# Performance work log

Hardware: AMD Instinct MI355X
Metric: run time of the kernel (lower is better)

The kernel has to match this reference:

```python
import jax, jax.numpy as jnp
import numpy as np

EMBED = 1024
HIDDEN = 4 * EMBED
EPS = 1e-5

def _layer_norm(x, g, b):
    mu = jnp.mean(x, axis=-1, keepdims=True)
    var = jnp.mean((x - mu) ** 2, axis=-1, keepdims=True)
    return (x - mu) * jax.lax.rsqrt(var + EPS) * g + b

def setup_inputs() -> dict:
    key = jax.random.key(0)
    ks = jax.random.split(key, 8)
    s = 1.0 / np.sqrt(EMBED)
    inp = {
        "x": jax.random.normal(ks[0], (4, 2048, EMBED), dtype=jnp.float32),
        "Wq": jax.random.normal(ks[1], (EMBED, EMBED), dtype=jnp.float32) * s,
        "bq": jnp.zeros((EMBED,), jnp.float32),
        "Wk": jax.random.normal(ks[2], (EMBED, EMBED), dtype=jnp.float32) * s,
        "bk": jnp.zeros((EMBED,), jnp.float32),
        "Wv": jax.random.normal(ks[3], (EMBED, EMBED), dtype=jnp.float32) * s,
        "bv": jnp.zeros((EMBED,), jnp.float32),
        "W1": jax.random.normal(ks[4], (EMBED, HIDDEN), dtype=jnp.float32) * s,
        "b1": jnp.zeros((HIDDEN,), jnp.float32),
        "W2": jax.random.normal(ks[5], (HIDDEN, EMBED), dtype=jnp.float32) * (1.0 / np.sqrt(HIDDEN)),
        "b2": jnp.zeros((EMBED,), jnp.float32),
        "g1": jnp.ones((EMBED,), jnp.float32),
        "be1": jnp.zeros((EMBED,), jnp.float32),
        "g2": jnp.ones((EMBED,), jnp.float32),
        "be2": jnp.zeros((EMBED,), jnp.float32),
    }
    return inp

def reference(x, Wq, bq, Wk, bk, Wv, bv, W1, b1, W2, b2, g1, be1, g2, be2):
    # pre-norm attention
    h = _layer_norm(x, g1, be1)
    Q = h @ Wq + bq  # [B,S,D]
    K = h @ Wk + bk
    V = h @ Wv + bv
    scale = 1.0 / jnp.sqrt(jnp.asarray(EMBED, x.dtype))
    scores = jnp.einsum('bqd,bkd->bqk', Q, K) * scale  # [B,S,S]
    weights = jax.nn.softmax(scores, axis=-1)
    attn = jnp.einsum('bqk,bkd->bqd', weights, V)
    x = x + attn
    # pre-norm MLP
    h2 = _layer_norm(x, g2, be2)
    ff = jax.nn.relu(h2 @ W1 + b1) @ W2 + b2
    return x + ff
```

## Files before the change

### kernel.cpp

```cpp
#include <hip/hip_runtime.h>

#define EMBED 1024
#define HID   4096
#define NB    4
#define SEQ   2048

typedef __attribute__((ext_vector_type(8))) __bf16 bf16x8;
typedef __attribute__((ext_vector_type(4))) float  f32x4;
typedef __attribute__((ext_vector_type(4))) int    i32x4;
typedef unsigned short u16;

__device__ __forceinline__ u16 f2bf(float f) {
  unsigned u = __float_as_uint(f);
  u += 0x7FFFu + ((u >> 16) & 1u);
  return (u16)(u >> 16);
}

typedef const __attribute__((address_space(1))) unsigned int* gas_t;
typedef __attribute__((address_space(3))) unsigned int* las_t;
__device__ __forceinline__ void gld16(const void* g, void* l) {
  __builtin_amdgcn_global_load_lds((gas_t)g, (las_t)l, 16, 0, 0);
}

#define RD16(p)       __builtin_bit_cast(bf16x8, *(const i32x4*)(p))
#define MFMA16(a,b,c) __builtin_amdgcn_mfma_f32_16x16x32_bf16(a, b, c, 0, 0, 0)
#define SCHED0()      __builtin_amdgcn_sched_barrier(0)
#define BARR()        __builtin_amdgcn_s_barrier()
#define LGKM(n)       asm volatile("s_waitcnt lgkmcnt(" #n ")" ::: "memory")
#define VMW(n)        asm volatile("s_waitcnt vmcnt(" #n ")" ::: "memory")

template<int EPI>
__global__ __launch_bounds__(512, 2) void gemm256(
    const u16* __restrict__ A, int lda, long long astr,
    const u16* __restrict__ B, int ldb, long long bstr,
    void* __restrict__ C, int ldc, long long cstr,
    const float* __restrict__ bias,
    const float* __restrict__ add,
    float scale, int Kdim)
{
  __shared__ char lds[131072];

  const int tid  = threadIdx.x;
  const int lane = tid & 63;
  const int w    = tid >> 6;
  const int wr   = w >> 2, wc = w & 3;
  const int l15  = lane & 15, l4 = lane >> 4;

  const int gx   = gridDim.x;
  const int nwg  = gx * gridDim.y;
  const int orig = blockIdx.y * gx + blockIdx.x;
  const int t    = ((nwg & 7) == 0) ? ((orig & 7) * (nwg >> 3) + (orig >> 3)) : orig;
  const int bx   = t % gx, by = t / gx;

  const u16* Ab = A + (size_t)blockIdx.z * astr + (size_t)by * 256 * lda;
  const u16* Bb = B + (size_t)blockIdx.z * bstr + (size_t)bx * 256 * ldb;

  const int    srow = tid >> 3;
  const size_t sa   = (size_t)srow * lda + (size_t)(((tid & 7) ^ (srow & 7)) * 8);
  const size_t sb   = (size_t)srow * ldb + (size_t)(((tid & 7) ^ (srow & 7)) * 8);
  const int    ldst = tid * 16;

  auto stA = [&](int buf, int q, int kk) {
    gld16(Ab + (size_t)(q * 64) * lda + kk + sa, lds + buf * 65536 + q * 8192 + ldst);
  };
  auto stB = [&](int buf, int i, int kk) {
    gld16(Bb + (size_t)(i * 64) * ldb + kk + sb, lds + buf * 65536 + 32768 + i * 8192 + ldst);
  };

  const int arow = (wr * 128 + l15) * 128;
  const int brow = 32768 + (wc * 64 + l15) * 128;
  const int cp0  = ((0 + l4) ^ (l15 & 7)) * 16;
  const int cp1  = ((4 + l4) ^ (l15 & 7)) * 16;

  f32x4 acc[8][4] = {};
  bf16x8 a0, a1, a2, a3, b0, b1, b2, b3, b4, b5, b6, b7;

  const int NT = Kdim >> 6;
  const int NI = NT >> 1;

#define BLOADS(LB) \
    b0 = RD16((LB) + brow + 0 * 2048 + cp0); \
    b1 = RD16((LB) + brow + 1 * 2048 + cp0); \
    b2 = RD16((LB) + brow + 2 * 2048 + cp0); \
    b3 = RD16((LB) + brow + 3 * 2048 + cp0); \
    b4 = RD16((LB) + brow + 0 * 2048 + cp1); \
    b5 = RD16((LB) + brow + 1 * 2048 + cp1); \
    b6 = RD16((LB) + brow + 2 * 2048 + cp1); \
    b7 = RD16((LB) + brow + 3 * 2048 + cp1);

#define PHASE(LB, MP, PRE, STG, VMST) do { \
    a0 = RD16((LB) + arow + (MP) * 4096 + cp0); \
    a1 = RD16((LB) + arow + (MP) * 4096 + cp1); \
    a2 = RD16((LB) + arow + (MP) * 4096 + 2048 + cp0); \
    a3 = RD16((LB) + arow + (MP) * 4096 + 2048 + cp1); \
    PRE STG VMST \
    SCHED0(); BARR(); LGKM(0); SCHED0(); \
    __builtin_amdgcn_s_setprio(1); \
    acc[2*(MP)  ][0] = MFMA16(a0, b0, acc[2*(MP)  ][0]); \
    acc[2*(MP)  ][1] = MFMA16(a0, b1, acc[2*(MP)  ][1]); \
    acc[2*(MP)  ][2] = MFMA16(a0, b2, acc[2*(MP)  ][2]); \
    acc[2*(MP)  ][3] = MFMA16(a0, b3, acc[2*(MP)  ][3]); \
    acc[2*(MP)+1][0] = MFMA16(a2, b0, acc[2*(MP)+1][0]); \
    acc[2*(MP)+1][1] = MFMA16(a2, b1, acc[2*(MP)+1][1]); \
    acc[2*(MP)+1][2] = MFMA16(a2, b2, acc[2*(MP)+1][2]); \
    acc[2*(MP)+1][3] = MFMA16(a2, b3, acc[2*(MP)+1][3]); \
    acc[2*(MP)  ][0] = MFMA16(a1, b4, acc[2*(MP)  ][0]); \
    acc[2*(MP)  ][1] = MFMA16(a1, b5, acc[2*(MP)  ][1]); \
    acc[2*(MP)  ][2] = MFMA16(a1, b6, acc[2*(MP)  ][2]); \
    acc[2*(MP)  ][3] = MFMA16(a1, b7, acc[2*(MP)  ][3]); \
    acc[2*(MP)+1][0] = MFMA16(a3, b4, acc[2*(MP)+1][0]); \
    acc[2*(MP)+1][1] = MFMA16(a3, b5, acc[2*(MP)+1][1]); \
    acc[2*(MP)+1][2] = MFMA16(a3, b6, acc[2*(MP)+1][2]); \
    acc[2*(MP)+1][3] = MFMA16(a3, b7, acc[2*(MP)+1][3]); \
    __builtin_amdgcn_s_setprio(0); \
    SCHED0(); BARR(); SCHED0(); \
  } while (0)

  stB(0, 0, 0); stB(0, 1, 0); stB(0, 2, 0); stB(0, 3, 0);
  stA(0, 0, 0); stA(0, 1, 0); stA(0, 2, 0); stA(0, 3, 0);
  stB(1, 0, 64); stB(1, 1, 64); stB(1, 2, 64); stB(1, 3, 64);
  stA(1, 0, 64); stA(1, 2, 64);
  VMW(6);
  BARR(); SCHED0();

  const char* L0 = lds;
  const char* L1 = lds + 65536;

  for (int I = 0; I < NI; ++I) {
    const bool st = (I + 1 < NI);
    const int k1 = (2 * I + 1) * 64;
    const int k2 = (2 * I + 2) * 64;
    const int k3 = (2 * I + 3) * 64;

    PHASE(L0, 0, BLOADS(L0), { stA(1, 1, k1); stA(1, 3, k1); }, ;);
    PHASE(L0, 1, ;, if (st) { stB(0, 0, k2); stB(0, 1, k2); }, ;);
    PHASE(L0, 2, ;, if (st) { stB(0, 2, k2); stB(0, 3, k2); }, ;);
    if (st) { PHASE(L0, 3, ;, { stA(0, 0, k2); stA(0, 2, k2); }, VMW(6);); }
    else    { PHASE(L0, 3, ;, ;, VMW(0);); }
    PHASE(L1, 0, BLOADS(L1), if (st) { stA(0, 1, k2); stA(0, 3, k2); }, ;);
    PHASE(L1, 1, ;, if (st) { stB(1, 0, k3); stB(1, 1, k3); }, ;);
    PHASE(L1, 2, ;, if (st) { stB(1, 2, k3); stB(1, 3, k3); }, ;);
    if (st) { PHASE(L1, 3, ;, { stA(1, 0, k3); stA(1, 2, k3); }, VMW(6);); }
    else    { PHASE(L1, 3, ;, ;, ;); }
  }
#undef PHASE
#undef BLOADS

  const int bm0 = by * 256 + wr * 128;
  const int bn0 = bx * 256 + wc * 64;
  float* Cf = (float*)C;
  u16*   Ch = (u16*)C;
  #pragma unroll
  for (int mi = 0; mi < 8; ++mi) {
    #pragma unroll
    for (int ni = 0; ni < 4; ++ni) {
      const int col = bn0 + ni * 16 + l15;
      const int r0  = bm0 + mi * 16 + l4 * 4;
      float bv = 0.f;
      if (EPI == 0 || EPI == 3 || EPI == 4) bv = bias[col];
      #pragma unroll
      for (int r = 0; r < 4; ++r) {
        const size_t idx = (size_t)blockIdx.z * cstr + (size_t)(r0 + r) * ldc + col;
        const float v = acc[mi][ni][r];
        if      (EPI == 0) Ch[idx] = f2bf(v + bv);
        else if (EPI == 1) Cf[idx] = v * scale;
        else if (EPI == 3) Ch[idx] = f2bf(fmaxf(v + bv, 0.f));
        else if (EPI == 4) Cf[idx] = v + bv + add[idx];
      }
    }
  }
}

template<int EPI>
__global__ __launch_bounds__(512, 2) void gemm8p(
    const u16* __restrict__ A, int lda, long long astr,
    const u16* __restrict__ B, int ldb, long long bstr,
    void* __restrict__ C, int ldc, long long cstr,
    const float* __restrict__ bias,
    const float* __restrict__ add,
    float scale, int Kdim)
{
  __shared__ i32x4 lds4[9216];
  const int SLOT = 49152;

  const int tid  = threadIdx.x;
  const int lane = tid & 63;
  const int w    = tid >> 6;
  const int wr   = w >> 1, wc = w & 1;
  const int l15  = lane & 15, l4 = lane >> 4;

  const int gx   = gridDim.x;
  const int nwg  = gx * gridDim.y;
  const int orig = blockIdx.y * gx + blockIdx.x;
  const int t    = ((nwg & 7) == 0) ? ((orig & 7) * (nwg >> 3) + (orig >> 3)) : orig;
  const int bx   = t % gx, by = t / gx;

  const u16* Ab = A + (size_t)blockIdx.z * astr + (size_t)by * 256 * lda;
  const u16* Bb = B + (size_t)blockIdx.z * bstr + (size_t)bx * 128 * ldb;

  size_t gaoff[4], gboff[2];
  #pragma unroll
  for (int i = 0; i < 4; ++i) {
    const int idx = i * 512 + tid, row = idx >> 3, gc = (idx & 7) ^ (row & 7);
    gaoff[i] = (size_t)row * lda + gc * 8;
  }
  #pragma unroll
  for (int j = 0; j < 2; ++j) {
    const int idx = j * 512 + tid, row = idx >> 3, gc = (idx & 7) ^ (row & 7);
    gboff[j] = (size_t)row * ldb + gc * 8;
  }

  int aoff[4], boff[4], cp16[2];
  #pragma unroll
  for (int m = 0; m < 4; ++m) aoff[m] = (wr * 64 + m * 16 + l15) * 128;
  #pragma unroll
  for (int n = 0; n < 4; ++n) boff[n] = 32768 + (wc * 64 + n * 16 + l15) * 128;
  cp16[0] = ((0 + l4) ^ (l15 & 7)) * 16;
  cp16[1] = ((4 + l4) ^ (l15 & 7)) * 16;

  f32x4 acc[4][4] = {};
  const int NT = Kdim >> 6;
  char* lbase = (char*)lds4;

  {
    char* s0 = lbase;
    char* s1 = lbase + SLOT;
    #pragma unroll
    for (int i = 0; i < 4; ++i) gld16(Ab + gaoff[i],      s0 + (i * 512 + w * 64) * 16);
    #pragma unroll
    for (int j = 0; j < 2; ++j) gld16(Bb + gboff[j],      s0 + 32768 + (j * 512 + w * 64) * 16);
    #pragma unroll
    for (int i = 0; i < 4; ++i) gld16(Ab + gaoff[i] + 64, s1 + (i * 512 + w * 64) * 16);
    #pragma unroll
    for (int j = 0; j < 2; ++j) gld16(Bb + gboff[j] + 64, s1 + 32768 + (j * 512 + w * 64) * 16);
  }

  int s = 0;
  for (int T = 0; T < NT; ++T) {
    const bool st  = (T + 2 < NT);
    const size_t kk = (size_t)(T + 2) * 64;
    const char* rA = lbase + s * SLOT;
    char* wS = lbase + ((s + 2 >= 3) ? (s - 1) : (s + 2)) * SLOT;

    if (T == NT - 1) VMW(0);
    else             VMW(6);
    BARR();
    SCHED0();

    bf16x8 b0, b1, b2, b3, a0, a1;

    b0 = RD16(rA + boff[0] + cp16[0]);
    b1 = RD16(rA + boff[1] + cp16[0]);
    b2 = RD16(rA + boff[2] + cp16[0]);
    b3 = RD16(rA + boff[3] + cp16[0]);
    a0 = RD16(rA + aoff[0] + cp16[0]);
    a1 = RD16(rA + aoff[1] + cp16[0]);
    if (st) {
      gld16(Ab + gaoff[0] + kk, wS + (0 * 512 + w * 64) * 16);
      gld16(Ab + gaoff[1] + kk, wS + (1 * 512 + w * 64) * 16);
    }
    BARR();
    LGKM(0);
    SCHED0();
    __builtin_amdgcn_s_setprio(1);
    acc[0][0] = MFMA16(a0, b0, acc[0][0]);
    acc[0][1] = MFMA16(a0, b1, acc[0][1]);
    acc[0][2] = MFMA16(a0, b2, acc[0][2]);
    acc[0][3] = MFMA16(a0, b3, acc[0][3]);
    acc[1][0] = MFMA16(a1, b0, acc[1][0]);
    acc[1][1] = MFMA16(a1, b1, acc[1][1]);
    acc[1][2] = MFMA16(a1, b2, acc[1][2]);
    acc[1][3] = MFMA16(a1, b3, acc[1][3]);
    __builtin_amdgcn_s_setprio(0);

    a0 = RD16(rA + aoff[2] + cp16[0]);
    a1 = RD16(rA + aoff[3] + cp16[0]);
    if (st) {
      gld16(Ab + gaoff[2] + kk, wS + (2 * 512 + w * 64) * 16);
      gld16(Ab + gaoff[3] + kk, wS + (3 * 512 + w * 64) * 16);
    }
    BARR();
    LGKM(0);
    SCHED0();
    __builtin_amdgcn_s_setprio(1);
    acc[2][0] = MFMA16(a0, b0, acc[2][0]);
    acc[2][1] = MFMA16(a0, b1, acc[2][1]);
    acc[2][2] = MFMA16(a0, b2, acc[2][2]);
    acc[2][3] = MFMA16(a0, b3, acc[2][3]);
    acc[3][0] = MFMA16(a1, b0, acc[3][0]);
    acc[3][1] = MFMA16(a1, b1, acc[3][1]);
    acc[3][2] = MFMA16(a1, b2, acc[3][2]);
    acc[3][3] = MFMA16(a1, b3, acc[3][3]);
    __builtin_amdgcn_s_setprio(0);

    b0 = RD16(rA + boff[0] + cp16[1]);
    b1 = RD16(rA + boff[1] + cp16[1]);
    b2 = RD16(rA + boff[2] + cp16[1]);
    b3 = RD16(rA + boff[3] + cp16[1]);
    a0 = RD16(rA + aoff[0] + cp16[1]);
    a1 = RD16(rA + aoff[1] + cp16[1]);
    if (st) {
      gld16(Bb + gboff[0] + kk, wS + 32768 + (0 * 512 + w * 64) * 16);
    }
    BARR();
    LGKM(0);
    SCHED0();
    __builtin_amdgcn_s_setprio(1);
    acc[0][0] = MFMA16(a0, b0, acc[0][0]);
    acc[0][1] = MFMA16(a0, b1, acc[0][1]);
    acc[0][2] = MFMA16(a0, b2, acc[0][2]);
    acc[0][3] = MFMA16(a0, b3, acc[0][3]);
    acc[1][0] = MFMA16(a1, b0, acc[1][0]);
    acc[1][1] = MFMA16(a1, b1, acc[1][1]);
    acc[1][2] = MFMA16(a1, b2, acc[1][2]);
    acc[1][3] = MFMA16(a1, b3, acc[1][3]);
    __builtin_amdgcn_s_setprio(0);

    a0 = RD16(rA + aoff[2] + cp16[1]);
    a1 = RD16(rA + aoff[3] + cp16[1]);
    if (st) {
      gld16(Bb + gboff[1] + kk, wS + 32768 + (1 * 512 + w * 64) * 16);
    }
    BARR();
    LGKM(0);
    SCHED0();
    __builtin_amdgcn_s_setprio(1);
    acc[2][0] = MFMA16(a0, b0, acc[2][0]);
    acc[2][1] = MFMA16(a0, b1, acc[2][1]);
    acc[2][2] = MFMA16(a0, b2, acc[2][2]);
    acc[2][3] = MFMA16(a0, b3, acc[2][3]);
    acc[3][0] = MFMA16(a1, b0, acc[3][0]);
    acc[3][1] = MFMA16(a1, b1, acc[3][1]);
    acc[3][2] = MFMA16(a1, b2, acc[3][2]);
    acc[3][3] = MFMA16(a1, b3, acc[3][3]);
    __builtin_amdgcn_s_setprio(0);

    s = (s + 1 == 3) ? 0 : s + 1;
  }

  const int bm0 = by * 256 + wr * 64;
  const int bn0 = bx * 128 + wc * 64;
  float* Cf = (float*)C;
  u16*   Ch = (u16*)C;
  #pragma unroll
  for (int mi = 0; mi < 4; ++mi) {
    #pragma unroll
    for (int ni = 0; ni < 4; ++ni) {
      const int col = bn0 + ni * 16 + l15;
      const int r0  = bm0 + mi * 16 + l4 * 4;
      float bv = 0.f;
      if (EPI == 0 || EPI == 4) bv = bias[col];
      #pragma unroll
      for (int r = 0; r < 4; ++r) {
        const size_t idx = (size_t)blockIdx.z * cstr + (size_t)(r0 + r) * ldc + col;
        const float v = acc[mi][ni][r];
        if      (EPI == 0) Ch[idx] = f2bf(v + bv);
        else if (EPI == 1) Cf[idx] = v * scale;
        else if (EPI == 2) Cf[idx] = v + add[idx];
        else if (EPI == 4) Cf[idx] = v + bv + add[idx];
        else if (EPI == 5) Ch[idx] = f2bf(v + bias[r0 + r]);
      }
    }
  }
}

__global__ __launch_bounds__(256) void ln_kernel(
    const float* __restrict__ x, const float* __restrict__ g,
    const float* __restrict__ be, u16* __restrict__ out)
{
  const int row = blockIdx.x;
  const int tid = threadIdx.x;
  const float4 v = ((const float4*)(x + (size_t)row * EMBED))[tid];
  float s  = v.x + v.y + v.z + v.w;
  float s2 = v.x * v.x + v.y * v.y + v.z * v.z + v.w * v.w;
  #pragma unroll
  for (int m = 1; m < 64; m <<= 1) { s += __shfl_xor(s, m); s2 += __shfl_xor(s2, m); }
  __shared__ float ls[4], ls2[4];
  const int w = tid >> 6;
  if ((tid & 63) == 0) { ls[w] = s; ls2[w] = s2; }
  __syncthreads();
  s  = ls[0] + ls[1] + ls[2] + ls[3];
  s2 = ls2[0] + ls2[1] + ls2[2] + ls2[3];
  const float mu   = s * (1.f / EMBED);
  const float var  = s2 * (1.f / EMBED) - mu * mu;
  const float rstd = rsqrtf(var + 1e-5f);
  const float4 gv = ((const float4*)g)[tid];
  const float4 bv = ((const float4*)be)[tid];
  ushort4 o;
  o.x = f2bf((v.x - mu) * rstd * gv.x + bv.x);
  o.y = f2bf((v.y - mu) * rstd * gv.y + bv.y);
  o.z = f2bf((v.z - mu) * rstd * gv.z + bv.z);
  o.w = f2bf((v.w - mu) * rstd * gv.w + bv.w);
  ((ushort4*)(out + (size_t)row * EMBED))[tid] = o;
}

__global__ __launch_bounds__(256) void softmax_kernel(
    const float* __restrict__ S, u16* __restrict__ P)
{
  const int tid = threadIdx.x;
  const size_t base = ((size_t)blockIdx.y * SEQ + blockIdx.x) * SEQ;
  const float4* src = (const float4*)(S + base);
  float4 a = src[tid];
  float4 b = src[tid + 256];
  float m = fmaxf(fmaxf(fmaxf(a.x, a.y), fmaxf(a.z, a.w)),
                  fmaxf(fmaxf(b.x, b.y), fmaxf(b.z, b.w)));
  #pragma unroll
  for (int msk = 1; msk < 64; msk <<= 1) m = fmaxf(m, __shfl_xor(m, msk));
  __shared__ float red[8];
  const int w = tid >> 6;
  if ((tid & 63) == 0) red[w] = m;
  __syncthreads();
  m = fmaxf(fmaxf(red[0], red[1]), fmaxf(red[2], red[3]));
  a.x = __expf(a.x - m); a.y = __expf(a.y - m); a.z = __expf(a.z - m); a.w = __expf(a.w - m);
  b.x = __expf(b.x - m); b.y = __expf(b.y - m); b.z = __expf(b.z - m); b.w = __expf(b.w - m);
  float s = a.x + a.y + a.z + a.w + b.x + b.y + b.z + b.w;
  #pragma unroll
  for (int msk = 1; msk < 64; msk <<= 1) s += __shfl_xor(s, msk);
  if ((tid & 63) == 0) red[4 + w] = s;
  __syncthreads();
  s = red[4] + red[5] + red[6] + red[7];
  const float inv = 1.0f / s;
  ushort4 oa, ob;
  oa.x = f2bf(a.x * inv); oa.y = f2bf(a.y * inv); oa.z = f2bf(a.z * inv); oa.w = f2bf(a.w * inv);
  ob.x = f2bf(b.x * inv); ob.y = f2bf(b.y * inv); ob.z = f2bf(b.z * inv); ob.w = f2bf(b.w * inv);
  ushort4* dst = (ushort4*)(P + base);
  dst[tid]       = oa;
  dst[tid + 256] = ob;
}

__global__ void transpose_cast_f32(const float* __restrict__ W, u16* __restrict__ Wt,
                                   int K, int N)
{
  __shared__ float t[32][33];
  const int tx = threadIdx.x, ty = threadIdx.y;
  const int n0 = blockIdx.x * 32, k0 = blockIdx.y * 32;
  #pragma unroll
  for (int i = 0; i < 4; ++i)
    t[ty + i * 8][tx] = W[(size_t)(k0 + ty + i * 8) * N + n0 + tx];
  __syncthreads();
  #pragma unroll
  for (int i = 0; i < 4; ++i)
    Wt[(size_t)(n0 + ty + i * 8) * K + k0 + tx] = f2bf(t[tx][ty + i * 8]);
}

__global__ void concat_bias2(const float* __restrict__ a, const float* __restrict__ b,
                             float* __restrict__ o)
{
  const int i = blockIdx.x * 1024 + threadIdx.x;
  o[i] = (i < 1024) ? a[i] : b[i - 1024];
}

extern "C" void kernel_launch(void* const* d_in, const int* in_sizes, int n_in,
                              void* d_out, int out_size, void* d_ws, size_t ws_size,
                              hipStream_t stream)
{
  const float* x   = (const float*)d_in[0];
  const float* Wq  = (const float*)d_in[1];
  const float* bq  = (const float*)d_in[2];
  const float* Wk  = (const float*)d_in[3];
  const float* bk  = (const float*)d_in[4];
  const float* Wv  = (const float*)d_in[5];
  const float* bv  = (const float*)d_in[6];
  const float* W1  = (const float*)d_in[7];
  const float* b1  = (const float*)d_in[8];
  const float* W2  = (const float*)d_in[9];
  const float* b2  = (const float*)d_in[10];
  const float* g1  = (const float*)d_in[11];
  const float* be1 = (const float*)d_in[12];
  const float* g2  = (const float*)d_in[13];
  const float* be2 = (const float*)d_in[14];
  float* out = (float*)d_out;

  const size_t RD = (size_t)NB * SEQ * EMBED;

  char* base = (char*)d_ws;
  size_t o = 0;
  auto alloc = [&](size_t bytes) -> void* {
    o = (o + 255) & ~(size_t)255;
    void* p = base + o;
    o += bytes;
    return p;
  };

  u16*   wqkT = (u16*)alloc((size_t)2 * EMBED * EMBED * 2);
  u16*   wvT  = (u16*)alloc((size_t)EMBED * EMBED * 2);
  u16*   w1T  = (u16*)alloc((size_t)HID * EMBED * 2);
  u16*   w2T  = (u16*)alloc((size_t)EMBED * HID * 2);
  float* bqk  = (float*)alloc(2048 * 4);
  u16*   h    = (u16*)alloc(RD * 2);
  u16*   QKb  = (u16*)alloc(RD * 2 * 2);
  u16*   Vt   = (u16*)alloc(RD * 2);
  float* x2   = (float*)alloc(RD * 4);

  const size_t need_batched = o + (size_t)NB * SEQ * SEQ * 6 + 1024;
  const int NZ = (ws_size >= need_batched) ? NB : 1;
  float* Sbuf = (float*)alloc((size_t)NZ * SEQ * SEQ * 4);
  u16*   Pb   = (u16*)alloc((size_t)NZ * SEQ * SEQ * 2);
  u16*   ff   = (NZ == NB) ? (u16*)Sbuf
                           : (u16*)alloc((size_t)NB * SEQ * HID * 2);

  const dim3 blk(512);
  const dim3 tblk(32, 8);

  transpose_cast_f32<<<dim3(32, 32), tblk, 0, stream>>>(Wq, wqkT, EMBED, EMBED);
  transpose_cast_f32<<<dim3(32, 32), tblk, 0, stream>>>(Wk, wqkT + (size_t)EMBED * EMBED, EMBED, EMBED);
  transpose_cast_f32<<<dim3(32, 32), tblk, 0, stream>>>(Wv, wvT, EMBED, EMBED);
  transpose_cast_f32<<<dim3(HID / 32, EMBED / 32), tblk, 0, stream>>>(W1, w1T, EMBED, HID);
  transpose_cast_f32<<<dim3(EMBED / 32, HID / 32), tblk, 0, stream>>>(W2, w2T, HID, EMBED);
  concat_bias2<<<dim3(2), dim3(1024), 0, stream>>>(bq, bk, bqk);

  ln_kernel<<<dim3(NB * SEQ), dim3(256), 0, stream>>>(x, g1, be1, h);

  gemm8p<0><<<dim3(2048 / 128, NB * SEQ / 256, 1), blk, 0, stream>>>(
      h, EMBED, 0LL, wqkT, EMBED, 0LL, QKb, 2048, 0LL, bqk, nullptr, 1.f, EMBED);

  gemm8p<5><<<dim3(SEQ / 128, EMBED / 256, NB), blk, 0, stream>>>(
      wvT, EMBED, 0LL, h, EMBED, (long long)SEQ * EMBED,
      Vt, SEQ, (long long)EMBED * SEQ, bv, nullptr, 1.f, EMBED);

  for (int b = 0; b < NB; b += NZ) {
    const u16* Qp  = QKb + (size_t)b * SEQ * 2048;
    const u16* Kp  = Qp + 1024;
    const u16* Vtp = Vt + (size_t)b * EMBED * SEQ;
    float* x2p     = x2 + (size_t)b * SEQ * EMBED;
    const float* xp = x + (size_t)b * SEQ * EMBED;
    gemm8p<1><<<dim3(SEQ / 128, SEQ / 256, NZ), blk, 0, stream>>>(
        Qp, 2048, (long long)SEQ * 2048, Kp, 2048, (long long)SEQ * 2048,
        Sbuf, SEQ, (long long)SEQ * SEQ, nullptr, nullptr, 0.03125f, EMBED);
    softmax_kernel<<<dim3(SEQ, NZ), dim3(256), 0, stream>>>(Sbuf, Pb);
    gemm8p<2><<<dim3(EMBED / 128, SEQ / 256, NZ), blk, 0, stream>>>(
        Pb, SEQ, (long long)SEQ * SEQ, Vtp, SEQ, (long long)EMBED * SEQ,
        x2p, EMBED, (long long)SEQ * EMBED, nullptr, xp, 1.f, SEQ);
  }

  ln_kernel<<<dim3(NB * SEQ), dim3(256), 0, stream>>>(x2, g2, be2, h);

  gemm256<3><<<dim3(HID / 256, NB * SEQ / 256, 1), blk, 0, stream>>>(
      h, EMBED, 0LL, w1T, EMBED, 0LL, ff, HID, 0LL, b1, nullptr, 1.f, EMBED);
  gemm8p<4><<<dim3(EMBED / 128, NB * SEQ / 256, 1), blk, 0, stream>>>(
      ff, HID, 0LL, w2T, HID, 0LL, out, EMBED, 0LL, b2, x2, 1.f, HID);
}
```

Before: 341.6 us.

## Rewrite 256x256 GEMM with 32x32 MFMA and use it for QK, scores, FFN1

Replaces the 256x256-tile GEMM's 16x16x32 MFMA inner loop with 32x32x16 bf16 MFMAs. It rearranges the A-tile LDS layout, the swizzled fragment reads and the epilogue row mapping to match. The new kernel now also runs the fused QK projection and the attention score GEMM, which previously used the 256x128 kernel. Separately, the pre-MFMA barriers are dropped in the gemm8p phases and in the new kernel's phases. This cuts sync overhead and raises MFMA efficiency, but it may introduce LDS races if the remaining barriers do not fully order the async loads against the reads.

```diff
diff --git a/kernel.cpp b/kernel.cpp
--- a/kernel.cpp
+++ b/kernel.cpp
@@ -5,9 +5,10 @@
 #define NB    4
 #define SEQ   2048
 
-typedef __attribute__((ext_vector_type(8))) __bf16 bf16x8;
-typedef __attribute__((ext_vector_type(4))) float  f32x4;
-typedef __attribute__((ext_vector_type(4))) int    i32x4;
+typedef __attribute__((ext_vector_type(8)))  __bf16 bf16x8;
+typedef __attribute__((ext_vector_type(4)))  float  f32x4;
+typedef __attribute__((ext_vector_type(16))) float  f32x16;
+typedef __attribute__((ext_vector_type(4)))  int    i32x4;
 typedef unsigned short u16;
 
 __device__ __forceinline__ u16 f2bf(float f) {
@@ -24,18 +25,18 @@
 
 #define RD16(p)       __builtin_bit_cast(bf16x8, *(const i32x4*)(p))
 #define MFMA16(a,b,c) __builtin_amdgcn_mfma_f32_16x16x32_bf16(a, b, c, 0, 0, 0)
+#define MFMA32(a,b,c) __builtin_amdgcn_mfma_f32_32x32x16_bf16(a, b, c, 0, 0, 0)
 #define SCHED0()      __builtin_amdgcn_sched_barrier(0)
 #define BARR()        __builtin_amdgcn_s_barrier()
 #define LGKM(n)       asm volatile("s_waitcnt lgkmcnt(" #n ")" ::: "memory")
 #define VMW(n)        asm volatile("s_waitcnt vmcnt(" #n ")" ::: "memory")
 
 template<int EPI>
-__global__ __launch_bounds__(512, 2) void gemm256(
+__global__ __launch_bounds__(512, 2) void gemm256v2(
     const u16* __restrict__ A, int lda, long long astr,
     const u16* __restrict__ B, int ldb, long long bstr,
     void* __restrict__ C, int ldc, long long cstr,
     const float* __restrict__ bias,
-    const float* __restrict__ add,
     float scale, int Kdim)
 {
   __shared__ char lds[131072];
@@ -44,7 +45,7 @@
   const int lane = tid & 63;
   const int w    = tid >> 6;
   const int wr   = w >> 2, wc = w & 3;
-  const int l15  = lane & 15, l4 = lane >> 4;
+  const int l31  = lane & 31, l5 = lane >> 5;
 
   const int gx   = gridDim.x;
   const int nwg  = gx * gridDim.y;
@@ -55,66 +56,62 @@
   const u16* Ab = A + (size_t)blockIdx.z * astr + (size_t)by * 256 * lda;
   const u16* Bb = B + (size_t)blockIdx.z * bstr + (size_t)bx * 256 * ldb;
 
-  const int    srow = tid >> 3;
-  const size_t sa   = (size_t)srow * lda + (size_t)(((tid & 7) ^ (srow & 7)) * 8);
-  const size_t sb   = (size_t)srow * ldb + (size_t)(((tid & 7) ^ (srow & 7)) * 8);
-  const int    ldst = tid * 16;
-
-  auto stA = [&](int buf, int q, int kk) {
-    gld16(Ab + (size_t)(q * 64) * lda + kk + sa, lds + buf * 65536 + q * 8192 + ldst);
+  const int schunk = (tid & 7) ^ ((tid >> 3) & 7);
+  auto stA = [&](int buf, int p, int kk) {
+    const int grow = ((tid >> 8) << 7) + p * 32 + ((tid >> 3) & 31);
+    gld16(Ab + (size_t)grow * lda + kk + schunk * 8,
+          lds + buf * 65536 + p * 8192 + tid * 16);
   };
-  auto stB = [&](int buf, int i, int kk) {
-    gld16(Bb + (size_t)(i * 64) * ldb + kk + sb, lds + buf * 65536 + 32768 + i * 8192 + ldst);
+  auto stB = [&](int buf, int u, int kk) {
+    const int grow = u * 64 + (tid >> 3);
+    gld16(Bb + (size_t)grow * ldb + kk + schunk * 8,
+          lds + buf * 65536 + 32768 + u * 8192 + tid * 16);
   };
 
-  const int arow = (wr * 128 + l15) * 128;
-  const int brow = 32768 + (wc * 64 + l15) * 128;
-  const int cp0  = ((0 + l4) ^ (l15 & 7)) * 16;
-  const int cp1  = ((4 + l4) ^ (l15 & 7)) * 16;
-
-  f32x4 acc[8][4] = {};
-  bf16x8 a0, a1, a2, a3, b0, b1, b2, b3, b4, b5, b6, b7;
+  const int arow = (wr * 32 + l31) * 128;
+  const int brow = 32768 + (wc * 64 + l31) * 128;
+  const int cs0 = ((0 + l5) ^ (lane & 7)) * 16;
+  const int cs1 = ((2 + l5) ^ (lane & 7)) * 16;
+  const int cs2 = ((4 + l5) ^ (lane & 7)) * 16;
+  const int cs3 = ((6 + l5) ^ (lane & 7)) * 16;
+
+  f32x16 acc[4][2] = {};
+  bf16x8 bf[2][4];
+
+#define BR32(LB) \
+    bf[0][0] = RD16((LB) + brow + cs0); \
+    bf[0][1] = RD16((LB) + brow + cs1); \
+    bf[0][2] = RD16((LB) + brow + cs2); \
+    bf[0][3] = RD16((LB) + brow + cs3); \
+    bf[1][0] = RD16((LB) + brow + 4096 + cs0); \
+    bf[1][1] = RD16((LB) + brow + 4096 + cs1); \
+    bf[1][2] = RD16((LB) + brow + 4096 + cs2); \
+    bf[1][3] = RD16((LB) + brow + 4096 + cs3);
+
+#define PH32(LB, MF, STG, VMST) do { \
+    bf16x8 a0 = RD16((LB) + (MF) * 8192 + arow + cs0); \
+    bf16x8 a1 = RD16((LB) + (MF) * 8192 + arow + cs1); \
+    bf16x8 a2 = RD16((LB) + (MF) * 8192 + arow + cs2); \
+    bf16x8 a3 = RD16((LB) + (MF) * 8192 + arow + cs3); \
+    STG VMST \
+    LGKM(0); SCHED0(); \
+    __builtin_amdgcn_s_setprio(1); \
+    acc[MF][0] = MFMA32(a0, bf[0][0], acc[MF][0]); \
+    acc[MF][1] = MFMA32(a0, bf[1][0], acc[MF][1]); \
+    acc[MF][0] = MFMA32(a1, bf[0][1], acc[MF][0]); \
+    acc[MF][1] = MFMA32(a1, bf[1][1], acc[MF][1]); \
+    acc[MF][0] = MFMA32(a2, bf[0][2], acc[MF][0]); \
+    acc[MF][1] = MFMA32(a2, bf[1][2], acc[MF][1]); \
+    acc[MF][0] = MFMA32(a3, bf[0][3], acc[MF][0]); \
+    acc[MF][1] = MFMA32(a3, bf[1][3], acc[MF][1]); \
+    __builtin_amdgcn_s_setprio(0); \
+    SCHED0(); BARR(); \
+  } while (0)
 
   const int NT = Kdim >> 6;
   const int NI = NT >> 1;
-
-#define BLOADS(LB) \
-    b0 = RD16((LB) + brow + 0 * 2048 + cp0); \
-    b1 = RD16((LB) + brow + 1 * 2048 + cp0); \
-    b2 = RD16((LB) + brow + 2 * 2048 + cp0); \
-    b3 = RD16((LB) + brow + 3 * 2048 + cp0); \
-    b4 = RD16((LB) + brow + 0 * 2048 + cp1); \
-    b5 = RD16((LB) + brow + 1 * 2048 + cp1); \
-    b6 = RD16((LB) + brow + 2 * 2048 + cp1); \
-    b7 = RD16((LB) + brow + 3 * 2048 + cp1);
-
-#define PHASE(LB, MP, PRE, STG, VMST) do { \
-    a0 = RD16((LB) + arow + (MP) * 4096 + cp0); \
-    a1 = RD16((LB) + arow + (MP) * 4096 + cp1); \
-    a2 = RD16((LB) + arow + (MP) * 4096 + 2048 + cp0); \
-    a3 = RD16((LB) + arow + (MP) * 4096 + 2048 + cp1); \
-    PRE STG VMST \
-    SCHED0(); BARR(); LGKM(0); SCHED0(); \
-    __builtin_amdgcn_s_setprio(1); \
-    acc[2*(MP)  ][0] = MFMA16(a0, b0, acc[2*(MP)  ][0]); \
-    acc[2*(MP)  ][1] = MFMA16(a0, b1, acc[2*(MP)  ][1]); \
-    acc[2*(MP)  ][2] = MFMA16(a0, b2, acc[2*(MP)  ][2]); \
-    acc[2*(MP)  ][3] = MFMA16(a0, b3, acc[2*(MP)  ][3]); \
-    acc[2*(MP)+1][0] = MFMA16(a2, b0, acc[2*(MP)+1][0]); \
-    acc[2*(MP)+1][1] = MFMA16(a2, b1, acc[2*(MP)+1][1]); \
-    acc[2*(MP)+1][2] = MFMA16(a2, b2, acc[2*(MP)+1][2]); \
-    acc[2*(MP)+1][3] = MFMA16(a2, b3, acc[2*(MP)+1][3]); \
-    acc[2*(MP)  ][0] = MFMA16(a1, b4, acc[2*(MP)  ][0]); \
-    acc[2*(MP)  ][1] = MFMA16(a1, b5, acc[2*(MP)  ][1]); \
-    acc[2*(MP)  ][2] = MFMA16(a1, b6, acc[2*(MP)  ][2]); \
-    acc[2*(MP)  ][3] = MFMA16(a1, b7, acc[2*(MP)  ][3]); \
-    acc[2*(MP)+1][0] = MFMA16(a3, b4, acc[2*(MP)+1][0]); \
-    acc[2*(MP)+1][1] = MFMA16(a3, b5, acc[2*(MP)+1][1]); \
-    acc[2*(MP)+1][2] = MFMA16(a3, b6, acc[2*(MP)+1][2]); \
-    acc[2*(MP)+1][3] = MFMA16(a3, b7, acc[2*(MP)+1][3]); \
-    __builtin_amdgcn_s_setprio(0); \
-    SCHED0(); BARR(); SCHED0(); \
-  } while (0)
+  const char* L0 = lds;
+  const char* L1 = lds + 65536;
 
   stB(0, 0, 0); stB(0, 1, 0); stB(0, 2, 0); stB(0, 3, 0);
   stA(0, 0, 0); stA(0, 1, 0); stA(0, 2, 0); stA(0, 3, 0);
@@ -123,52 +120,51 @@
   VMW(6);
   BARR(); SCHED0();
 
-  const char* L0 = lds;
-  const char* L1 = lds + 65536;
-
   for (int I = 0; I < NI; ++I) {
     const bool st = (I + 1 < NI);
     const int k1 = (2 * I + 1) * 64;
     const int k2 = (2 * I + 2) * 64;
     const int k3 = (2 * I + 3) * 64;
 
-    PHASE(L0, 0, BLOADS(L0), { stA(1, 1, k1); stA(1, 3, k1); }, ;);
-    PHASE(L0, 1, ;, if (st) { stB(0, 0, k2); stB(0, 1, k2); }, ;);
-    PHASE(L0, 2, ;, if (st) { stB(0, 2, k2); stB(0, 3, k2); }, ;);
-    if (st) { PHASE(L0, 3, ;, { stA(0, 0, k2); stA(0, 2, k2); }, VMW(6);); }
-    else    { PHASE(L0, 3, ;, ;, VMW(0);); }
-    PHASE(L1, 0, BLOADS(L1), if (st) { stA(0, 1, k2); stA(0, 3, k2); }, ;);
-    PHASE(L1, 1, ;, if (st) { stB(1, 0, k3); stB(1, 1, k3); }, ;);
-    PHASE(L1, 2, ;, if (st) { stB(1, 2, k3); stB(1, 3, k3); }, ;);
-    if (st) { PHASE(L1, 3, ;, { stA(1, 0, k3); stA(1, 2, k3); }, VMW(6);); }
-    else    { PHASE(L1, 3, ;, ;, ;); }
-  }
-#undef PHASE
-#undef BLOADS
+    PH32(L0, 0, BR32(L0) { stA(1, 1, k1); stA(1, 3, k1); }, ;);
+    PH32(L0, 1, if (st) { stB(0, 0, k2); stB(0, 1, k2); }, ;);
+    PH32(L0, 2, if (st) { stB(0, 2, k2); stB(0, 3, k2); }, ;);
+    if (st) { PH32(L0, 3, { stA(0, 0, k2); stA(0, 2, k2); }, VMW(6);); }
+    else    { PH32(L0, 3, ;, VMW(0);); }
+    PH32(L1, 0, BR32(L1) if (st) { stA(0, 1, k2); stA(0, 3, k2); }, ;);
+    PH32(L1, 1, if (st) { stB(1, 0, k3); stB(1, 1, k3); }, ;);
+    PH32(L1, 2, if (st) { stB(1, 2, k3); stB(1, 3, k3); }, ;);
+    if (st) { PH32(L1, 3, { stA(1, 0, k3); stA(1, 2, k3); }, VMW(6);); }
+    else    { PH32(L1, 3, ;, ;); }
+  }
+#undef PH32
+#undef BR32
 
   const int bm0 = by * 256 + wr * 128;
   const int bn0 = bx * 256 + wc * 64;
+  const size_t zoff = (size_t)blockIdx.z * cstr;
   float* Cf = (float*)C;
   u16*   Ch = (u16*)C;
-  #pragma unroll
-  for (int mi = 0; mi < 8; ++mi) {
-    #pragma unroll
-    for (int ni = 0; ni < 4; ++ni) {
-      const int col = bn0 + ni * 16 + l15;
-      const int r0  = bm0 + mi * 16 + l4 * 4;
-      float bv = 0.f;
-      if (EPI == 0 || EPI == 3 || EPI == 4) bv = bias[col];
-      #pragma unroll
-      for (int r = 0; r < 4; ++r) {
-        const size_t idx = (size_t)blockIdx.z * cstr + (size_t)(r0 + r) * ldc + col;
-        const float v = acc[mi][ni][r];
-        if      (EPI == 0) Ch[idx] = f2bf(v + bv);
-        else if (EPI == 1) Cf[idx] = v * scale;
-        else if (EPI == 3) Ch[idx] = f2bf(fmaxf(v + bv, 0.f));
-        else if (EPI == 4) Cf[idx] = v + bv + add[idx];
-      }
-    }
-  }
+
+#define ST32(MF, NF) do { \
+    const int col = bn0 + (NF) * 32 + l31; \
+    const int rb  = bm0 + (MF) * 32 + l5 * 4; \
+    float bv = 0.f; \
+    if (EPI == 0 || EPI == 3) bv = bias[col]; \
+    _Pragma("unroll") \
+    for (int r = 0; r < 16; ++r) { \
+      const int row = rb + (r & 3) + ((r >> 2) << 3); \
+      const size_t idx = zoff + (size_t)row * ldc + col; \
+      const float v = acc[MF][NF][r]; \
+      if      (EPI == 0) Ch[idx] = f2bf(v + bv); \
+      else if (EPI == 1) Cf[idx] = v * scale; \
+      else if (EPI == 3) Ch[idx] = f2bf(fmaxf(v + bv, 0.f)); \
+    } \
+  } while (0)
+
+  ST32(0, 0); ST32(0, 1); ST32(1, 0); ST32(1, 1);
+  ST32(2, 0); ST32(2, 1); ST32(3, 0); ST32(3, 1);
+#undef ST32
 }
 
 template<int EPI>
@@ -259,7 +255,6 @@
       gld16(Ab + gaoff[0] + kk, wS + (0 * 512 + w * 64) * 16);
       gld16(Ab + gaoff[1] + kk, wS + (1 * 512 + w * 64) * 16);
     }
-    BARR();
     LGKM(0);
     SCHED0();
     __builtin_amdgcn_s_setprio(1);
@@ -279,7 +274,6 @@
       gld16(Ab + gaoff[2] + kk, wS + (2 * 512 + w * 64) * 16);
       gld16(Ab + gaoff[3] + kk, wS + (3 * 512 + w * 64) * 16);
     }
-    BARR();
     LGKM(0);
     SCHED0();
     __builtin_amdgcn_s_setprio(1);
@@ -302,7 +296,6 @@
     if (st) {
       gld16(Bb + gboff[0] + kk, wS + 32768 + (0 * 512 + w * 64) * 16);
     }
-    BARR();
     LGKM(0);
     SCHED0();
     __builtin_amdgcn_s_setprio(1);
@@ -321,7 +314,6 @@
     if (st) {
       gld16(Bb + gboff[1] + kk, wS + 32768 + (1 * 512 + w * 64) * 16);
     }
-    BARR();
     LGKM(0);
     SCHED0();
     __builtin_amdgcn_s_setprio(1);
@@ -511,8 +503,8 @@
 
   ln_kernel<<<dim3(NB * SEQ), dim3(256), 0, stream>>>(x, g1, be1, h);
 
-  gemm8p<0><<<dim3(2048 / 128, NB * SEQ / 256, 1), blk, 0, stream>>>(
-      h, EMBED, 0LL, wqkT, EMBED, 0LL, QKb, 2048, 0LL, bqk, nullptr, 1.f, EMBED);
+  gemm256v2<0><<<dim3(2048 / 256, NB * SEQ / 256, 1), blk, 0, stream>>>(
+      h, EMBED, 0LL, wqkT, EMBED, 0LL, QKb, 2048, 0LL, bqk, 1.f, EMBED);
 
   gemm8p<5><<<dim3(SEQ / 128, EMBED / 256, NB), blk, 0, stream>>>(
       wvT, EMBED, 0LL, h, EMBED, (long long)SEQ * EMBED,
@@ -524,9 +516,9 @@
     const u16* Vtp = Vt + (size_t)b * EMBED * SEQ;
     float* x2p     = x2 + (size_t)b * SEQ * EMBED;
     const float* xp = x + (size_t)b * SEQ * EMBED;
-    gemm8p<1><<<dim3(SEQ / 128, SEQ / 256, NZ), blk, 0, stream>>>(
+    gemm256v2<1><<<dim3(SEQ / 256, SEQ / 256, NZ), blk, 0, stream>>>(
         Qp, 2048, (long long)SEQ * 2048, Kp, 2048, (long long)SEQ * 2048,
-        Sbuf, SEQ, (long long)SEQ * SEQ, nullptr, nullptr, 0.03125f, EMBED);
+        Sbuf, SEQ, (long long)SEQ * SEQ, nullptr, 0.03125f, EMBED);
     softmax_kernel<<<dim3(SEQ, NZ), dim3(256), 0, stream>>>(Sbuf, Pb);
     gemm8p<2><<<dim3(EMBED / 128, SEQ / 256, NZ), blk, 0, stream>>>(
         Pb, SEQ, (long long)SEQ * SEQ, Vtp, SEQ, (long long)EMBED * SEQ,
@@ -535,8 +527,8 @@
 
   ln_kernel<<<dim3(NB * SEQ), dim3(256), 0, stream>>>(x2, g2, be2, h);
 
-  gemm256<3><<<dim3(HID / 256, NB * SEQ / 256, 1), blk, 0, stream>>>(
-      h, EMBED, 0LL, w1T, EMBED, 0LL, ff, HID, 0LL, b1, nullptr, 1.f, EMBED);
+  gemm256v2<3><<<dim3(HID / 256, NB * SEQ / 256, 1), blk, 0, stream>>>(
+      h, EMBED, 0LL, w1T, EMBED, 0LL, ff, HID, 0LL, b1, 1.f, EMBED);
   gemm8p<4><<<dim3(EMBED / 128, NB * SEQ / 256, 1), blk, 0, stream>>>(
       ff, HID, 0LL, w2T, HID, 0LL, out, EMBED, 0LL, b2, x2, 1.f, HID);
 }
```

Result: no change. 344.9 us (+1.0%).
